# Performance work log

Measured on AMD Instinct MI355X. Metric: run time of the kernel, lower is better.

Reference implementation:

```python
import jax, jax.numpy as jnp
import numpy as np

GAMMA = 0.99

def _get_D(gamma, T, dtype=jnp.float32):
    # D[n, m] = gamma**(n-m) if n >= m else 0 (NaN/inf cleanup as in torch source)
    n = jnp.arange(T)
    diff = n[:, None] - n[None, :]
    return jnp.where(diff >= 0, jnp.power(jnp.asarray(gamma, dtype), jnp.maximum(diff, 0).astype(dtype)), jnp.zeros((), dtype))

def setup_inputs() -> dict:
    key = jax.random.key(0)
    kX, kQ, kK, kV = jax.random.split(key, 4)
    B, T, I, C = 2, 4096, 1024, 1024
    X = jax.random.normal(kX, (B, T, I), dtype=jnp.float32)
    att_mask = jnp.ones((B, T), dtype=jnp.float32)
    S_n = jnp.zeros((B, C, C), dtype=jnp.float32)
    # params initialized as randn/I per the torch module
    W_Q = jax.random.normal(kQ, (I, C), dtype=jnp.float32) / I
    W_K = jax.random.normal(kK, (I, C), dtype=jnp.float32) / I
    W_V = jax.random.normal(kV, (I, I), dtype=jnp.float32) / I
    return {"X": X, "att_mask": att_mask, "S_n": S_n, "W_Q": W_Q, "W_K": W_K, "W_V": W_V}

def reference(X, att_mask, S_n, W_Q, W_K, W_V):
    # COINBlock.forward_parallel (dropout in eval mode = identity; att_mask unused)
    B, T, _ = X.shape
    C = W_Q.shape[1]
    Q = X @ W_Q            # [B,T,C]
    K = X @ W_K            # [B,T,C]
    V = X @ W_V            # [B,T,I]
    A = jnp.einsum('btc,bsc->bts', Q, K)          # [B,T,T]
    A = A * _get_D(GAMMA, T, X.dtype)[None, :, :]  # decay-masked scores
    out = A @ V                                    # [B,T,I]
    out = jnp.swapaxes(out, -2, -1).reshape(B, T, C)  # faithful transpose+view (I == C)
    return out, S_n
```

## Files before the change

### kernel.cpp

```cpp
#include <hip/hip_runtime.h>
#include <cstdint>
#include <cstddef>


using bf16x8 = __attribute__((ext_vector_type(8))) short;
using s16x4  = __attribute__((ext_vector_type(4))) short;
using f32x4  = __attribute__((ext_vector_type(4))) float;

#define T_SEQ 4096
#define C_DIM 1024

static constexpr float L2G = -0.0144995697f;

__device__ __forceinline__ short f2bf(float f) {
  unsigned u = __builtin_bit_cast(unsigned, f);
  u += 0x7FFFu + ((u >> 16) & 1u);
  return (short)(u >> 16);
}

__device__ __forceinline__ void async_ld16(const short* g, const short* l) {
  __builtin_amdgcn_global_load_lds(
      (const __attribute__((address_space(1))) unsigned int*)(uintptr_t)g,
      (__attribute__((address_space(3))) unsigned int*)(unsigned)(uintptr_t)l,
      16, 0, 0);
}

#define FENCE asm volatile("" ::: "memory")
#define BAR   do { FENCE; __builtin_amdgcn_s_barrier(); FENCE; } while (0)
#define VMC(N) asm volatile("s_waitcnt vmcnt(" #N ")" ::: "memory")

__device__ __forceinline__ void gemm8p(
    const short* __restrict__ A, const short* __restrict__ B,
    int lda, int ldb, int NT,
    short* __restrict__ lsA, short* __restrict__ lsB,
    f32x4 (&acc)[8][4])
{
  const int tid  = threadIdx.x;
  const int lane = tid & 63;
  const int wave = tid >> 6;
  const int wM   = wave >> 2;
  const int wN   = wave & 3;
  const int quad = lane >> 4;
  const int l15  = lane & 15;
  const int key  = l15 & 7;
  const int uk0  = (quad ^ key) * 8;
  const int uk1  = ((4 ^ quad) ^ key) * 8;
  const short* aB0 = lsA + wM * 8192 + l15 * 64 + uk0;
  const short* aB1 = lsA + wM * 8192 + l15 * 64 + uk1;
  const short* bB0 = lsB + wN * 4096 + l15 * 64 + uk0;
  const short* bB1 = lsB + wN * 4096 + l15 * 64 + uk1;
  const int rl0 = lane >> 3;
  const int cu  = ((lane & 7) ^ rl0) * 8;
  const short* pa[4];
  const short* pb[4];
#pragma unroll
  for (int j = 0; j < 4; ++j) {
    const int grow = (wave * 4 + j) * 8 + rl0;
    pa[j] = A + (size_t)grow * lda + cu;
    pb[j] = B + (size_t)grow * ldb + cu;
  }

#define ST_A8(SLOT, TT)                                                             \
  { _Pragma("unroll")                                                               \
    for (int j = 0; j < 4; ++j)                                                     \
      async_ld16(pa[j] + (size_t)(TT) * 64,                                         \
                 lsA + (SLOT) * 16384 + (wave * 4 + j) * 512 + lane * 8); }
#define ST_B8(SLOT, TT)                                                             \
  { _Pragma("unroll")                                                               \
    for (int j = 0; j < 4; ++j)                                                     \
      async_ld16(pb[j] + (size_t)(TT) * 64,                                         \
                 lsB + (SLOT) * 16384 + (wave * 4 + j) * 512 + lane * 8); }

  bf16x8 af03k0[4], af03k1[4], af47k0[4], af47k1[4], bfk0[4], bfk1[4];

  ST_A8(0, 0);
  ST_B8(0, 0);
  ST_B8(1, 1);
  VMC(4);
  BAR;
#pragma unroll
  for (int mi = 0; mi < 4; ++mi) af03k0[mi] = *(const bf16x8*)(aB0 + mi * 1024);
#pragma unroll
  for (int ni = 0; ni < 4; ++ni) bfk0[ni]   = *(const bf16x8*)(bB0 + ni * 1024);

  for (int t = 0; t < NT; ++t) {
    const int sA = (t & 1) * 16384;
    const int sB = (t & 1) * 16384;

#pragma unroll
    for (int mi = 0; mi < 4; ++mi) af03k1[mi] = *(const bf16x8*)(aB1 + sA + mi * 1024);
#pragma unroll
    for (int ni = 0; ni < 4; ++ni) bfk1[ni]   = *(const bf16x8*)(bB1 + sB + ni * 1024);
    if (t + 1 < NT) ST_A8((t + 1) & 1, t + 1);
    __builtin_amdgcn_s_setprio(1);
#pragma unroll
    for (int mi = 0; mi < 4; ++mi)
#pragma unroll
      for (int ni = 0; ni < 4; ++ni)
        acc[mi][ni] = __builtin_amdgcn_mfma_f32_16x16x32_bf16(
            af03k0[mi], bfk0[ni], acc[mi][ni], 0, 0, 0);
    __builtin_amdgcn_s_setprio(0);
    BAR;

#pragma unroll
    for (int mi = 0; mi < 4; ++mi) af47k0[mi] = *(const bf16x8*)(aB0 + sA + 4096 + mi * 1024);
    __builtin_amdgcn_s_setprio(1);
#pragma unroll
    for (int mi = 0; mi < 4; ++mi)
#pragma unroll
      for (int ni = 0; ni < 4; ++ni)
        acc[mi][ni] = __builtin_amdgcn_mfma_f32_16x16x32_bf16(
            af03k1[mi], bfk1[ni], acc[mi][ni], 0, 0, 0);
    __builtin_amdgcn_s_setprio(0);
    BAR;

#pragma unroll
    for (int mi = 0; mi < 4; ++mi) af47k1[mi] = *(const bf16x8*)(aB1 + sA + 4096 + mi * 1024);
    if (t + 2 < NT) ST_B8(t & 1, t + 2);
    __builtin_amdgcn_s_setprio(1);
#pragma unroll
    for (int mi = 0; mi < 4; ++mi)
#pragma unroll
      for (int ni = 0; ni < 4; ++ni)
        acc[4 + mi][ni] = __builtin_amdgcn_mfma_f32_16x16x32_bf16(
            af47k0[mi], bfk0[ni], acc[4 + mi][ni], 0, 0, 0);
    __builtin_amdgcn_s_setprio(0);
    if (t + 2 < NT) VMC(4); else VMC(0);
    BAR;

    if (t + 1 < NT) {
      const int sA2 = ((t + 1) & 1) * 16384;
      const int sB2 = ((t + 1) & 1) * 16384;
#pragma unroll
      for (int mi = 0; mi < 4; ++mi) af03k0[mi] = *(const bf16x8*)(aB0 + sA2 + mi * 1024);
#pragma unroll
      for (int ni = 0; ni < 4; ++ni) bfk0[ni]   = *(const bf16x8*)(bB0 + sB2 + ni * 1024);
    }
    __builtin_amdgcn_s_setprio(1);
#pragma unroll
    for (int mi = 0; mi < 4; ++mi)
#pragma unroll
      for (int ni = 0; ni < 4; ++ni)
        acc[4 + mi][ni] = __builtin_amdgcn_mfma_f32_16x16x32_bf16(
            af47k1[mi], bfk1[ni], acc[4 + mi][ni], 0, 0, 0);
    __builtin_amdgcn_s_setprio(0);
    BAR;
  }
#undef ST_A8
#undef ST_B8
}

__device__ __forceinline__ void gemm4p3(
    const short* __restrict__ A, const short* __restrict__ B,
    int lda, int ldb, int NT,
    short* __restrict__ lsA, short* __restrict__ lsB,
    f32x4 (&acc)[4][4])
{
  const int tid  = threadIdx.x;
  const int lane = tid & 63;
  const int wave = tid >> 6;
  const int wM   = wave >> 1;
  const int wN   = wave & 1;
  const int quad = lane >> 4;
  const int l15  = lane & 15;
  const int key  = l15 & 7;
  const int uk0  = (quad ^ key) * 8;
  const int uk1  = ((4 ^ quad) ^ key) * 8;
  const short* aR0 = lsA + (wM * 64 + l15) * 64 + uk0;
  const short* aR1 = lsA + (wM * 64 + l15) * 64 + uk1;
  const short* bR0 = lsB + (wN * 64 + l15) * 64 + uk0;
  const short* bR1 = lsB + (wN * 64 + l15) * 64 + uk1;
  const int rl0 = lane >> 3;
  const int cu  = ((lane & 7) ^ rl0) * 8;
  const short* pa[2][2];
  const short* pb[2][2];
#pragma unroll
  for (int u = 0; u < 2; ++u)
#pragma unroll
    for (int j = 0; j < 2; ++j) {
      pa[u][j] = A + (size_t)(u * 64 + (wave + 4 * j) * 8 + rl0) * lda + cu;
      pb[u][j] = B + (size_t)(u * 64 + (wave + 4 * j) * 8 + rl0) * ldb + cu;
    }

#define S4A(SLOT, TT)                                                               \
  { _Pragma("unroll")                                                               \
    for (int u = 0; u < 2; ++u)                                                     \
      _Pragma("unroll")                                                             \
      for (int j = 0; j < 2; ++j)                                                   \
        async_ld16(pa[u][j] + (size_t)(TT) * 64,                                    \
                   lsA + (SLOT) * 8192 + u * 4096 + (wave + 4 * j) * 512 + lane * 8); }
#define S4B(SLOT, TT)                                                               \
  { _Pragma("unroll")                                                               \
    for (int u = 0; u < 2; ++u)                                                     \
      _Pragma("unroll")                                                             \
      for (int j = 0; j < 2; ++j)                                                   \
        async_ld16(pb[u][j] + (size_t)(TT) * 64,                                    \
                   lsB + (SLOT) * 8192 + u * 4096 + (wave + 4 * j) * 512 + lane * 8); }

  bf16x8 afA[4][2], afB[4][2], b01A[2][2], b01B[2][2], b23[2][2];

#define RD_AF(DST, SLOT)                                                            \
  { _Pragma("unroll")                                                               \
    for (int i = 0; i < 4; ++i) {                                                   \
      DST[i][0] = *(const bf16x8*)(aR0 + (SLOT) * 8192 + i * 1024);                 \
      DST[i][1] = *(const bf16x8*)(aR1 + (SLOT) * 8192 + i * 1024);                 \
    } }
#define RD_B01(DST, SLOT)                                                           \
  { _Pragma("unroll")                                                               \
    for (int n = 0; n < 2; ++n) {                                                   \
      DST[n][0] = *(const bf16x8*)(bR0 + (SLOT) * 8192 + n * 1024);                 \
      DST[n][1] = *(const bf16x8*)(bR1 + (SLOT) * 8192 + n * 1024);                 \
    } }
#define RD_B23(SLOT)                                                                \
  { _Pragma("unroll")                                                               \
    for (int n = 0; n < 2; ++n) {                                                   \
      b23[n][0] = *(const bf16x8*)(bR0 + (SLOT) * 8192 + (2 + n) * 1024);           \
      b23[n][1] = *(const bf16x8*)(bR1 + (SLOT) * 8192 + (2 + n) * 1024);           \
    } }
#define MFLO(AF, B01)                                                               \
  { __builtin_amdgcn_s_setprio(1);                                                  \
    _Pragma("unroll")                                                               \
    for (int kk = 0; kk < 2; ++kk)                                                  \
      _Pragma("unroll")                                                             \
      for (int i = 0; i < 4; ++i)                                                   \
        _Pragma("unroll")                                                           \
        for (int n = 0; n < 2; ++n)                                                 \
          acc[i][n] = __builtin_amdgcn_mfma_f32_16x16x32_bf16(                      \
              AF[i][kk], B01[n][kk], acc[i][n], 0, 0, 0);                           \
    __builtin_amdgcn_s_setprio(0); }
#define MFHI(AF)                                                                    \
  { __builtin_amdgcn_s_setprio(1);                                                  \
    _Pragma("unroll")                                                               \
    for (int kk = 0; kk < 2; ++kk)                                                  \
      _Pragma("unroll")                                                             \
      for (int i = 0; i < 4; ++i)                                                   \
        _Pragma("unroll")                                                           \
        for (int n = 0; n < 2; ++n)                                                 \
          acc[i][2 + n] = __builtin_amdgcn_mfma_f32_16x16x32_bf16(                  \
              AF[i][kk], b23[n][kk], acc[i][2 + n], 0, 0, 0);                       \
    __builtin_amdgcn_s_setprio(0); }

  S4A(0, 0); S4B(0, 0); S4A(1, 1); S4B(1, 1);
  VMC(8);
  BAR;
  RD_AF(afA, 0);
  RD_B01(b01A, 0);

  int s0 = 0;
  for (int tp = 0; tp < NT; tp += 2) {
    int s1 = s0 + 1; if (s1 == 3) s1 = 0;
    int s2 = s1 + 1; if (s2 == 3) s2 = 0;
    const int s3 = s0;
    const bool g2 = (tp + 2 < NT);
    const bool g3 = (tp + 3 < NT);

    RD_B23(s0);
    if (g2) S4A(s2, tp + 2);
    MFLO(afA, b01A);
    if (g2) VMC(4); else VMC(0);
    BAR;
    RD_AF(afB, s1);
    RD_B01(b01B, s1);
    if (g2) S4B(s2, tp + 2);
    MFHI(afA);
    if (g2) VMC(4); else VMC(0);
    BAR;
    RD_B23(s1);
    if (g3) S4A(s3, tp + 3);
    MFLO(afB, b01B);
    if (g3) VMC(4); else VMC(0);
    BAR;
    if (g2) { RD_AF(afA, s2); RD_B01(b01A, s2); }
    if (g3) S4B(s3, tp + 3);
    MFHI(afB);
    if (g3) VMC(4); else VMC(0);
    BAR;

    s0 = s2;
  }
#undef S4A
#undef S4B
#undef RD_AF
#undef RD_B01
#undef RD_B23
#undef MFLO
#undef MFHI
}


__global__ __launch_bounds__(256) void k_convX(const float* __restrict__ x,
                                               short* __restrict__ y) {
  const size_t i = ((size_t)blockIdx.x * 256 + threadIdx.x) * 4;
  const float4 v = *(const float4*)(x + i);
  s16x4 o;
  o[0] = f2bf(v.x); o[1] = f2bf(v.y); o[2] = f2bf(v.z); o[3] = f2bf(v.w);
  *(s16x4*)(y + i) = o;
}

__global__ __launch_bounds__(256) void k_convWt(const float* __restrict__ Wq,
                                                const float* __restrict__ Wk,
                                                const float* __restrict__ Wv,
                                                short* __restrict__ Wtq,
                                                short* __restrict__ Wtk,
                                                short* __restrict__ Wtv) {
  const float* W = (blockIdx.z == 0) ? Wq : (blockIdx.z == 1) ? Wk : Wv;
  short* Wt      = (blockIdx.z == 0) ? Wtq : (blockIdx.z == 1) ? Wtk : Wtv;
  __shared__ float t[32][33];
  const int tx = threadIdx.x & 31;
  const int ty = threadIdx.x >> 5;
  const int bc = blockIdx.x * 32;
  const int bi = blockIdx.y * 32;
#pragma unroll
  for (int j = 0; j < 32; j += 8)
    t[ty + j][tx] = W[(size_t)(bi + ty + j) * 1024 + bc + tx];
  __syncthreads();
#pragma unroll
  for (int j = 0; j < 32; j += 8)
    Wt[(size_t)(bc + ty + j) * 1024 + bi + tx] = f2bf(t[tx][ty + j]);
}


__global__ __launch_bounds__(512, 1) void k_proj(
    const short* __restrict__ Xb, const short* __restrict__ Wtq,
    const short* __restrict__ Wtk, const short* __restrict__ Wtv,
    short* __restrict__ Qb, short* __restrict__ Kb, short* __restrict__ Vt) {
  __shared__ short lsA[2 * 16384];
  __shared__ short lsB[2 * 16384];
  f32x4 acc[8][4];
#pragma unroll
  for (int i = 0; i < 8; ++i)
#pragma unroll
    for (int j = 0; j < 4; ++j) acc[i][j] = 0.f;

  const int z  = blockIdx.y;
  const int bx = blockIdx.x;
  const short* Ab;
  const short* Bb;
  int m, n;
  if (z < 2) {
    m = bx >> 2; n = bx & 3;
    Ab = Xb + (size_t)m * 256 * 1024;
    Bb = (z ? Wtk : Wtq) + (size_t)n * 256 * 1024;
  } else {
    m = bx >> 5; n = bx & 31;
    Ab = Wtv + (size_t)m * 256 * 1024;
    Bb = Xb + (size_t)n * 256 * 1024;
  }
  gemm8p(Ab, Bb, 1024, 1024, 16, lsA, lsB, acc);

  const int lane = threadIdx.x & 63, wave = threadIdx.x >> 6;
  const int wM = wave >> 2, wN = wave & 3;
  const int quad = lane >> 4, l15 = lane & 15;
  if (z < 2) {
    short* O = z ? Kb : Qb;
#pragma unroll
    for (int mi = 0; mi < 8; ++mi)
#pragma unroll
      for (int ni = 0; ni < 4; ++ni)
#pragma unroll
        for (int r = 0; r < 4; ++r) {
          const int row = m * 256 + wM * 128 + mi * 16 + quad * 4 + r;
          const int col = n * 256 + wN * 64 + ni * 16 + l15;
          O[(size_t)row * 1024 + col] = f2bf(acc[mi][ni][r]);
        }
  } else {
#pragma unroll
    for (int mi = 0; mi < 8; ++mi)
#pragma unroll
      for (int ni = 0; ni < 4; ++ni)
#pragma unroll
        for (int r = 0; r < 4; ++r) {
          const int crow = m * 256 + wM * 128 + mi * 16 + quad * 4 + r;
          const int t8   = n * 256 + wN * 64 + ni * 16 + l15;
          const int b = t8 >> 12, tt = t8 & 4095;
          Vt[(size_t)b * C_DIM * T_SEQ + (size_t)crow * T_SEQ + tt] =
              f2bf(acc[mi][ni][r]);
        }
  }
}

__global__ __launch_bounds__(512, 1) void k_scores(const short* __restrict__ Qb,
                                                   const short* __restrict__ Kb,
                                                   short* __restrict__ P) {
  __shared__ short lsA[2 * 16384];
  __shared__ short lsB[2 * 16384];
  f32x4 acc[8][4];
#pragma unroll
  for (int i = 0; i < 8; ++i)
#pragma unroll
    for (int j = 0; j < 4; ++j) acc[i][j] = 0.f;

  int id = blockIdx.x, mm = 0;
  while (id >= 16 - mm) { id -= 16 - mm; ++mm; }
  const int nn = mm + id;

  const size_t b = blockIdx.y;
  const short* Ab = Qb + b * T_SEQ * C_DIM + (size_t)nn * 256 * 1024;
  const short* Bb = Kb + b * T_SEQ * C_DIM + (size_t)mm * 256 * 1024;
  gemm8p(Ab, Bb, 1024, 1024, 16, lsA, lsB, acc);

  short* Pb = P + b * (size_t)T_SEQ * T_SEQ;
  const int lane = threadIdx.x & 63, wave = threadIdx.x >> 6;
  const int wM = wave >> 2, wN = wave & 3;
  const int quad = lane >> 4, l15 = lane & 15;
#pragma unroll
  for (int mi = 0; mi < 8; ++mi)
#pragma unroll
    for (int ni = 0; ni < 4; ++ni)
#pragma unroll
      for (int r = 0; r < 4; ++r) {
        const int n = nn * 256 + wM * 128 + mi * 16 + quad * 4 + r;
        const int m = mm * 256 + wN * 64 + ni * 16 + l15;
        float v = 0.f;
        if (n >= m) v = acc[mi][ni][r] * exp2f((float)(n - m) * L2G);
        Pb[(size_t)n * T_SEQ + m] = f2bf(v);
      }
}

__global__ __launch_bounds__(256, 1) void k_pv(const short* __restrict__ Vt,
                                               const short* __restrict__ P,
                                               float* __restrict__ out) {
  __shared__ short lsA[3 * 8192];
  __shared__ short lsB[3 * 8192];
  const int p  = blockIdx.x;
  const int iy = blockIdx.y;
  const size_t b = blockIdx.z;

  const short* Ab = Vt + b * (size_t)C_DIM * T_SEQ + (size_t)iy * 128 * T_SEQ;
  const short* Pb = P + b * (size_t)T_SEQ * T_SEQ;
  float* Ob = out + b * (size_t)C_DIM * T_SEQ;

  const int lane = threadIdx.x & 63, wave = threadIdx.x >> 6;
  const int wM = wave >> 1, wN = wave & 1;
  const int quad = lane >> 4, l15 = lane & 15;

  const int cols[2] = { 31 - p, p };
#pragma unroll
  for (int cc = 0; cc < 2; ++cc) {
    const int c = cols[cc];
    f32x4 acc[4][4];
#pragma unroll
    for (int i = 0; i < 4; ++i)
#pragma unroll
      for (int j = 0; j < 4; ++j) acc[i][j] = 0.f;
    gemm4p3(Ab, Pb + (size_t)c * 128 * T_SEQ, T_SEQ, T_SEQ, 2 * c + 2,
            lsA, lsB, acc);
#pragma unroll
    for (int mi = 0; mi < 4; ++mi)
#pragma unroll
      for (int ni = 0; ni < 4; ++ni)
#pragma unroll
        for (int r = 0; r < 4; ++r) {
          const int irow = iy * 128 + wM * 64 + mi * 16 + quad * 4 + r;
          const int tcol = c * 128 + wN * 64 + ni * 16 + l15;
          Ob[(size_t)irow * T_SEQ + tcol] = acc[mi][ni][r];
        }
  }
}


extern "C" void kernel_launch(void* const* d_in, const int* in_sizes, int n_in,
                              void* d_out, int out_size, void* d_ws, size_t ws_size,
                              hipStream_t stream) {
  const float* X  = (const float*)d_in[0];
  const float* Wq = (const float*)d_in[3];
  const float* Wk = (const float*)d_in[4];
  const float* Wv = (const float*)d_in[5];
  float* out = (float*)d_out;

  char* ws = (char*)d_ws;
  short* Xb  = (short*)(ws);
  short* Wtq = (short*)(ws + 16777216);
  short* Wtk = (short*)(ws + 18874368);
  short* Wtv = (short*)(ws + 20971520);
  short* Qb  = (short*)(ws + 23068672);
  short* Kb  = (short*)(ws + 39845888);
  short* Vt  = (short*)(ws + 56623104);
  short* P   = (short*)(ws + 73400320);

  const size_t mainN = (size_t)2 * T_SEQ * C_DIM;
  hipMemsetAsync((char*)d_out + mainN * 4, 0,
                 ((size_t)out_size - mainN) * 4, stream);

  k_convX  <<<dim3(8192),       dim3(256), 0, stream>>>(X, Xb);
  k_convWt <<<dim3(32, 32, 3),  dim3(256), 0, stream>>>(Wq, Wk, Wv, Wtq, Wtk, Wtv);
  k_proj   <<<dim3(128, 3),     dim3(512), 0, stream>>>(Xb, Wtq, Wtk, Wtv, Qb, Kb, Vt);
  k_scores <<<dim3(136, 2),     dim3(512), 0, stream>>>(Qb, Kb, P);
  k_pv     <<<dim3(16, 8, 2),   dim3(256), 0, stream>>>(Vt, P, out);
}
```

Baseline: 286.7 us.

## Switch projection and score GEMMs to 128x128 tiles with 3-stage B pipeline

Replaces the 256x256, 8-wave GEMM core used by the projection and score kernels with a new 128x128, 4-wave core. It keeps A double-buffered and B triple-buffered, and processes two K-steps per loop iteration. Grids grow to 512x3 and 528x2 blocks with two blocks per CU, which improves load balance over the 256 CUs and wave-level occupancy. The cost is lower per-block data reuse, so more global and LDS traffic per FLOP, plus a more intricate slot-rotation schedule.

After: 269.3 us. 1.06x faster.

```diff
diff --git a/kernel.cpp b/kernel.cpp
--- a/kernel.cpp
+++ b/kernel.cpp
@@ -29,125 +29,142 @@
 #define BAR   do { FENCE; __builtin_amdgcn_s_barrier(); FENCE; } while (0)
 #define VMC(N) asm volatile("s_waitcnt vmcnt(" #N ")" ::: "memory")
 
-__device__ __forceinline__ void gemm8p(
+
+__device__ __forceinline__ void gemm4p2(
     const short* __restrict__ A, const short* __restrict__ B,
     int lda, int ldb, int NT,
     short* __restrict__ lsA, short* __restrict__ lsB,
-    f32x4 (&acc)[8][4])
+    f32x4 (&acc)[4][4])
 {
   const int tid  = threadIdx.x;
   const int lane = tid & 63;
   const int wave = tid >> 6;
-  const int wM   = wave >> 2;
-  const int wN   = wave & 3;
+  const int wM   = wave >> 1;
+  const int wN   = wave & 1;
   const int quad = lane >> 4;
   const int l15  = lane & 15;
   const int key  = l15 & 7;
   const int uk0  = (quad ^ key) * 8;
   const int uk1  = ((4 ^ quad) ^ key) * 8;
-  const short* aB0 = lsA + wM * 8192 + l15 * 64 + uk0;
-  const short* aB1 = lsA + wM * 8192 + l15 * 64 + uk1;
-  const short* bB0 = lsB + wN * 4096 + l15 * 64 + uk0;
-  const short* bB1 = lsB + wN * 4096 + l15 * 64 + uk1;
+  const short* aR0 = lsA + (wM * 64 + l15) * 64 + uk0;
+  const short* aR1 = lsA + (wM * 64 + l15) * 64 + uk1;
+  const short* bR0 = lsB + (wN * 64 + l15) * 64 + uk0;
+  const short* bR1 = lsB + (wN * 64 + l15) * 64 + uk1;
   const int rl0 = lane >> 3;
   const int cu  = ((lane & 7) ^ rl0) * 8;
-  const short* pa[4];
-  const short* pb[4];
-#pragma unroll
-  for (int j = 0; j < 4; ++j) {
-    const int grow = (wave * 4 + j) * 8 + rl0;
-    pa[j] = A + (size_t)grow * lda + cu;
-    pb[j] = B + (size_t)grow * ldb + cu;
+  const short* pa[2][2];
+  const short* pb[2][2];
+#pragma unroll
+  for (int u = 0; u < 2; ++u)
+#pragma unroll
+    for (int j = 0; j < 2; ++j) {
+      pa[u][j] = A + (size_t)(u * 64 + (wave + 4 * j) * 8 + rl0) * lda + cu;
+      pb[u][j] = B + (size_t)(u * 64 + (wave + 4 * j) * 8 + rl0) * ldb + cu;
+    }
+
+#define S4A(SLOT, TT)                                                               \
+  { _Pragma("unroll")                                                               \
+    for (int u = 0; u < 2; ++u)                                                     \
+      _Pragma("unroll")                                                             \
+      for (int j = 0; j < 2; ++j)                                                   \
+        async_ld16(pa[u][j] + (size_t)(TT) * 64,                                    \
+                   lsA + (SLOT) * 8192 + u * 4096 + (wave + 4 * j) * 512 + lane * 8); }
+#define S4B(SLOT, TT)                                                               \
+  { _Pragma("unroll")                                                               \
+    for (int u = 0; u < 2; ++u)                                                     \
+      _Pragma("unroll")                                                             \
+      for (int j = 0; j < 2; ++j)                                                   \
+        async_ld16(pb[u][j] + (size_t)(TT) * 64,                                    \
+                   lsB + (SLOT) * 8192 + u * 4096 + (wave + 4 * j) * 512 + lane * 8); }
+
+  bf16x8 afA[4][2], afB[4][2], b01A[2][2], b01B[2][2], b23[2][2];
+
+#define RD_AF(DST, SLOT)                                                            \
+  { _Pragma("unroll")                                                               \
+    for (int i = 0; i < 4; ++i) {                                                   \
+      DST[i][0] = *(const bf16x8*)(aR0 + (SLOT) * 8192 + i * 1024);                 \
+      DST[i][1] = *(const bf16x8*)(aR1 + (SLOT) * 8192 + i * 1024);                 \
+    } }
+#define RD_B01(DST, SLOT)                                                           \
+  { _Pragma("unroll")                                                               \
+    for (int n = 0; n < 2; ++n) {                                                   \
+      DST[n][0] = *(const bf16x8*)(bR0 + (SLOT) * 8192 + n * 1024);                 \
+      DST[n][1] = *(const bf16x8*)(bR1 + (SLOT) * 8192 + n * 1024);                 \
+    } }
+#define RD_B23(SLOT)                                                                \
+  { _Pragma("unroll")                                                               \
+    for (int n = 0; n < 2; ++n) {                                                   \
+      b23[n][0] = *(const bf16x8*)(bR0 + (SLOT) * 8192 + (2 + n) * 1024);           \
+      b23[n][1] = *(const bf16x8*)(bR1 + (SLOT) * 8192 + (2 + n) * 1024);           \
+    } }
+#define MFLO(AF, B01)                                                               \
+  { __builtin_amdgcn_s_setprio(1);                                                  \
+    _Pragma("unroll")                                                               \
+    for (int kk = 0; kk < 2; ++kk)                                                  \
+      _Pragma("unroll")                                                             \
+      for (int i = 0; i < 4; ++i)                                                   \
+        _Pragma("unroll")                                                           \
+        for (int n = 0; n < 2; ++n)                                                 \
+          acc[i][n] = __builtin_amdgcn_mfma_f32_16x16x32_bf16(                      \
+              AF[i][kk], B01[n][kk], acc[i][n], 0, 0, 0);                           \
+    __builtin_amdgcn_s_setprio(0); }
+#define MFHI(AF)                                                                    \
+  { __builtin_amdgcn_s_setprio(1);                                                  \
+    _Pragma("unroll")                                                               \
+    for (int kk = 0; kk < 2; ++kk)                                                  \
+      _Pragma("unroll")                                                             \
+      for (int i = 0; i < 4; ++i)                                                   \
+        _Pragma("unroll")                                                           \
+        for (int n = 0; n < 2; ++n)                                                 \
+          acc[i][2 + n] = __builtin_amdgcn_mfma_f32_16x16x32_bf16(                  \
+              AF[i][kk], b23[n][kk], acc[i][2 + n], 0, 0, 0);                       \
+    __builtin_amdgcn_s_setprio(0); }
+
+  S4A(0, 0); S4B(0, 0); S4A(1, 1); S4B(1, 1);
+  VMC(8);
+  BAR;
+  RD_AF(afA, 0);
+  RD_B01(b01A, 0);
+
+  int s0 = 0;
+  for (int tp = 0; tp < NT; tp += 2) {
+    int s1 = s0 + 1; if (s1 == 3) s1 = 0;
+    int s2 = s1 + 1; if (s2 == 3) s2 = 0;
+    const int s3 = s0;
+    const bool g2 = (tp + 2 < NT);
+    const bool g3 = (tp + 3 < NT);
+
+    RD_B23(s0);
+    if (g2) S4B(s2, tp + 2);
+    MFLO(afA, b01A);
+    if (g2) VMC(4); else VMC(0);
+    BAR;
+    RD_AF(afB, 1);
+    RD_B01(b01B, s1);
+    if (g2) S4A(0, tp + 2);
+    MFHI(afA);
+    if (g2) VMC(4); else VMC(0);
+    BAR;
+    RD_B23(s1);
+    if (g3) S4B(s3, tp + 3);
+    MFLO(afB, b01B);
+    if (g3) VMC(4); else VMC(0);
+    BAR;
+    if (g2) { RD_AF(afA, 0); RD_B01(b01A, s2); }
+    if (g3) S4A(1, tp + 3);
+    MFHI(afB);
+    if (g3) VMC(4); else VMC(0);
+    BAR;
+
+    s0 = s2;
   }
-
-#define ST_A8(SLOT, TT)                                                             \
-  { _Pragma("unroll")                                                               \
-    for (int j = 0; j < 4; ++j)                                                     \
-      async_ld16(pa[j] + (size_t)(TT) * 64,                                         \
-                 lsA + (SLOT) * 16384 + (wave * 4 + j) * 512 + lane * 8); }
-#define ST_B8(SLOT, TT)                                                             \
-  { _Pragma("unroll")                                                               \
-    for (int j = 0; j < 4; ++j)                                                     \
-      async_ld16(pb[j] + (size_t)(TT) * 64,                                         \
-                 lsB + (SLOT) * 16384 + (wave * 4 + j) * 512 + lane * 8); }
-
-  bf16x8 af03k0[4], af03k1[4], af47k0[4], af47k1[4], bfk0[4], bfk1[4];
-
-  ST_A8(0, 0);
-  ST_B8(0, 0);
-  ST_B8(1, 1);
-  VMC(4);
-  BAR;
-#pragma unroll
-  for (int mi = 0; mi < 4; ++mi) af03k0[mi] = *(const bf16x8*)(aB0 + mi * 1024);
-#pragma unroll
-  for (int ni = 0; ni < 4; ++ni) bfk0[ni]   = *(const bf16x8*)(bB0 + ni * 1024);
-
-  for (int t = 0; t < NT; ++t) {
-    const int sA = (t & 1) * 16384;
-    const int sB = (t & 1) * 16384;
-
-#pragma unroll
-    for (int mi = 0; mi < 4; ++mi) af03k1[mi] = *(const bf16x8*)(aB1 + sA + mi * 1024);
-#pragma unroll
-    for (int ni = 0; ni < 4; ++ni) bfk1[ni]   = *(const bf16x8*)(bB1 + sB + ni * 1024);
-    if (t + 1 < NT) ST_A8((t + 1) & 1, t + 1);
-    __builtin_amdgcn_s_setprio(1);
-#pragma unroll
-    for (int mi = 0; mi < 4; ++mi)
-#pragma unroll
-      for (int ni = 0; ni < 4; ++ni)
-        acc[mi][ni] = __builtin_amdgcn_mfma_f32_16x16x32_bf16(
-            af03k0[mi], bfk0[ni], acc[mi][ni], 0, 0, 0);
-    __builtin_amdgcn_s_setprio(0);
-    BAR;
-
-#pragma unroll
-    for (int mi = 0; mi < 4; ++mi) af47k0[mi] = *(const bf16x8*)(aB0 + sA + 4096 + mi * 1024);
-    __builtin_amdgcn_s_setprio(1);
-#pragma unroll
-    for (int mi = 0; mi < 4; ++mi)
-#pragma unroll
-      for (int ni = 0; ni < 4; ++ni)
-        acc[mi][ni] = __builtin_amdgcn_mfma_f32_16x16x32_bf16(
-            af03k1[mi], bfk1[ni], acc[mi][ni], 0, 0, 0);
-    __builtin_amdgcn_s_setprio(0);
-    BAR;
-
-#pragma unroll
-    for (int mi = 0; mi < 4; ++mi) af47k1[mi] = *(const bf16x8*)(aB1 + sA + 4096 + mi * 1024);
-    if (t + 2 < NT) ST_B8(t & 1, t + 2);
-    __builtin_amdgcn_s_setprio(1);
-#pragma unroll
-    for (int mi = 0; mi < 4; ++mi)
-#pragma unroll
-      for (int ni = 0; ni < 4; ++ni)
-        acc[4 + mi][ni] = __builtin_amdgcn_mfma_f32_16x16x32_bf16(
-            af47k0[mi], bfk0[ni], acc[4 + mi][ni], 0, 0, 0);
-    __builtin_amdgcn_s_setprio(0);
-    if (t + 2 < NT) VMC(4); else VMC(0);
-    BAR;
-
-    if (t + 1 < NT) {
-      const int sA2 = ((t + 1) & 1) * 16384;
-      const int sB2 = ((t + 1) & 1) * 16384;
-#pragma unroll
-      for (int mi = 0; mi < 4; ++mi) af03k0[mi] = *(const bf16x8*)(aB0 + sA2 + mi * 1024);
-#pragma unroll
-      for (int ni = 0; ni < 4; ++ni) bfk0[ni]   = *(const bf16x8*)(bB0 + sB2 + ni * 1024);
-    }
-    __builtin_amdgcn_s_setprio(1);
-#pragma unroll
-    for (int mi = 0; mi < 4; ++mi)
-#pragma unroll
-      for (int ni = 0; ni < 4; ++ni)
-        acc[4 + mi][ni] = __builtin_amdgcn_mfma_f32_16x16x32_bf16(
-            af47k1[mi], bfk1[ni], acc[4 + mi][ni], 0, 0, 0);
-    __builtin_amdgcn_s_setprio(0);
-    BAR;
-  }
-#undef ST_A8
-#undef ST_B8
+#undef S4A
+#undef S4B
+#undef RD_AF
+#undef RD_B01
+#undef RD_B23
+#undef MFLO
+#undef MFHI
 }
 
 __device__ __forceinline__ void gemm4p3(
@@ -320,15 +337,15 @@
 }
 
 
-__global__ __launch_bounds__(512, 1) void k_proj(
+__global__ __launch_bounds__(256, 2) void k_proj(
     const short* __restrict__ Xb, const short* __restrict__ Wtq,
     const short* __restrict__ Wtk, const short* __restrict__ Wtv,
     short* __restrict__ Qb, short* __restrict__ Kb, short* __restrict__ Vt) {
-  __shared__ short lsA[2 * 16384];
-  __shared__ short lsB[2 * 16384];
-  f32x4 acc[8][4];
-#pragma unroll
-  for (int i = 0; i < 8; ++i)
+  __shared__ short lsA[2 * 8192];
+  __shared__ short lsB[3 * 8192];
+  f32x4 acc[4][4];
+#pragma unroll
+  for (int i = 0; i < 4; ++i)
 #pragma unroll
     for (int j = 0; j < 4; ++j) acc[i][j] = 0.f;
 
@@ -338,40 +355,40 @@
   const short* Bb;
   int m, n;
   if (z < 2) {
-    m = bx >> 2; n = bx & 3;
-    Ab = Xb + (size_t)m * 256 * 1024;
-    Bb = (z ? Wtk : Wtq) + (size_t)n * 256 * 1024;
+    m = bx >> 3; n = bx & 7;
+    Ab = Xb + (size_t)m * 128 * 1024;
+    Bb = (z ? Wtk : Wtq) + (size_t)n * 128 * 1024;
   } else {
-    m = bx >> 5; n = bx & 31;
-    Ab = Wtv + (size_t)m * 256 * 1024;
-    Bb = Xb + (size_t)n * 256 * 1024;
+    m = bx >> 6; n = bx & 63;
+    Ab = Wtv + (size_t)m * 128 * 1024;
+    Bb = Xb + (size_t)n * 128 * 1024;
   }
-  gemm8p(Ab, Bb, 1024, 1024, 16, lsA, lsB, acc);
+  gemm4p2(Ab, Bb, 1024, 1024, 16, lsA, lsB, acc);
 
   const int lane = threadIdx.x & 63, wave = threadIdx.x >> 6;
-  const int wM = wave >> 2, wN = wave & 3;
+  const int wM = wave >> 1, wN = wave & 1;
   const int quad = lane >> 4, l15 = lane & 15;
   if (z < 2) {
     short* O = z ? Kb : Qb;
 #pragma unroll
-    for (int mi = 0; mi < 8; ++mi)
+    for (int mi = 0; mi < 4; ++mi)
 #pragma unroll
       for (int ni = 0; ni < 4; ++ni)
 #pragma unroll
         for (int r = 0; r < 4; ++r) {
-          const int row = m * 256 + wM * 128 + mi * 16 + quad * 4 + r;
-          const int col = n * 256 + wN * 64 + ni * 16 + l15;
+          const int row = m * 128 + wM * 64 + mi * 16 + quad * 4 + r;
+          const int col = n * 128 + wN * 64 + ni * 16 + l15;
           O[(size_t)row * 1024 + col] = f2bf(acc[mi][ni][r]);
         }
   } else {
 #pragma unroll
-    for (int mi = 0; mi < 8; ++mi)
+    for (int mi = 0; mi < 4; ++mi)
 #pragma unroll
       for (int ni = 0; ni < 4; ++ni)
 #pragma unroll
         for (int r = 0; r < 4; ++r) {
-          const int crow = m * 256 + wM * 128 + mi * 16 + quad * 4 + r;
-          const int t8   = n * 256 + wN * 64 + ni * 16 + l15;
+          const int crow = m * 128 + wM * 64 + mi * 16 + quad * 4 + r;
+          const int t8   = n * 128 + wN * 64 + ni * 16 + l15;
           const int b = t8 >> 12, tt = t8 & 4095;
           Vt[(size_t)b * C_DIM * T_SEQ + (size_t)crow * T_SEQ + tt] =
               f2bf(acc[mi][ni][r]);
@@ -379,38 +396,38 @@
   }
 }
 
-__global__ __launch_bounds__(512, 1) void k_scores(const short* __restrict__ Qb,
+__global__ __launch_bounds__(256, 2) void k_scores(const short* __restrict__ Qb,
                                                    const short* __restrict__ Kb,
                                                    short* __restrict__ P) {
-  __shared__ short lsA[2 * 16384];
-  __shared__ short lsB[2 * 16384];
-  f32x4 acc[8][4];
-#pragma unroll
-  for (int i = 0; i < 8; ++i)
+  __shared__ short lsA[2 * 8192];
+  __shared__ short lsB[3 * 8192];
+  f32x4 acc[4][4];
+#pragma unroll
+  for (int i = 0; i < 4; ++i)
 #pragma unroll
     for (int j = 0; j < 4; ++j) acc[i][j] = 0.f;
 
   int id = blockIdx.x, mm = 0;
-  while (id >= 16 - mm) { id -= 16 - mm; ++mm; }
+  while (id >= 32 - mm) { id -= 32 - mm; ++mm; }
   const int nn = mm + id;
 
   const size_t b = blockIdx.y;
-  const short* Ab = Qb + b * T_SEQ * C_DIM + (size_t)nn * 256 * 1024;
-  const short* Bb = Kb + b * T_SEQ * C_DIM + (size_t)mm * 256 * 1024;
-  gemm8p(Ab, Bb, 1024, 1024, 16, lsA, lsB, acc);
+  const short* Ab = Qb + b * T_SEQ * C_DIM + (size_t)nn * 128 * 1024;
+  const short* Bb = Kb + b * T_SEQ * C_DIM + (size_t)mm * 128 * 1024;
+  gemm4p2(Ab, Bb, 1024, 1024, 16, lsA, lsB, acc);
 
   short* Pb = P + b * (size_t)T_SEQ * T_SEQ;
   const int lane = threadIdx.x & 63, wave = threadIdx.x >> 6;
-  const int wM = wave >> 2, wN = wave & 3;
+  const int wM = wave >> 1, wN = wave & 1;
   const int quad = lane >> 4, l15 = lane & 15;
 #pragma unroll
-  for (int mi = 0; mi < 8; ++mi)
+  for (int mi = 0; mi < 4; ++mi)
 #pragma unroll
     for (int ni = 0; ni < 4; ++ni)
 #pragma unroll
       for (int r = 0; r < 4; ++r) {
-        const int n = nn * 256 + wM * 128 + mi * 16 + quad * 4 + r;
-        const int m = mm * 256 + wN * 64 + ni * 16 + l15;
+        const int n = nn * 128 + wM * 64 + mi * 16 + quad * 4 + r;
+        const int m = mm * 128 + wN * 64 + ni * 16 + l15;
         float v = 0.f;
         if (n >= m) v = acc[mi][ni][r] * exp2f((float)(n - m) * L2G);
         Pb[(size_t)n * T_SEQ + m] = f2bf(v);
@@ -484,7 +501,7 @@
 
   k_convX  <<<dim3(8192),       dim3(256), 0, stream>>>(X, Xb);
   k_convWt <<<dim3(32, 32, 3),  dim3(256), 0, stream>>>(Wq, Wk, Wv, Wtq, Wtk, Wtv);
-  k_proj   <<<dim3(128, 3),     dim3(512), 0, stream>>>(Xb, Wtq, Wtk, Wtv, Qb, Kb, Vt);
-  k_scores <<<dim3(136, 2),     dim3(512), 0, stream>>>(Qb, Kb, P);
+  k_proj   <<<dim3(512, 3),     dim3(256), 0, stream>>>(Xb, Wtq, Wtk, Wtv, Qb, Kb, Vt);
+  k_scores <<<dim3(528, 2),     dim3(256), 0, stream>>>(Qb, Kb, P);
   k_pv     <<<dim3(16, 8, 2),   dim3(256), 0, stream>>>(Vt, P, out);
 }
```
